# Optimization experiments

Measured on AMD Instinct MI355X. Metric: run time of the kernel, lower is better.

Reference implementation:

```python
import jax, jax.numpy as jnp
import numpy as np

HEADS = 16
D_MODEL = 1024
EXPANSION = 2
D_EXP = D_MODEL * EXPANSION          # 2048
D_HEAD = D_EXP // HEADS              # 128
B, SEQ = 1, 2048
LN_EPS = 1e-5
NEG_BIG = -1e10


def layer_norm(x, w, b):
    mu = jnp.mean(x, axis=-1, keepdims=True)
    var = jnp.var(x, axis=-1, keepdims=True)
    return (x - mu) * jax.lax.rsqrt(var + LN_EPS) * w + b


def setup_inputs() -> dict:
    key = jax.random.key(0)
    ks = jax.random.split(key, 8)
    d_out = 4 * D_EXP + HEADS  # merged fanout linear: q,k,v,p (D_EXP each) + y (HEADS)
    x = jax.random.normal(ks[0], (B, SEQ, D_MODEL), dtype=jnp.float32)
    W_in = 0.02 * jax.random.normal(ks[1], (d_out, D_MODEL), dtype=jnp.float32)
    b_in = jnp.zeros((d_out,), dtype=jnp.float32)
    # position head init from module: weight zeros, bias linspace(-8,8,heads)
    W_in = W_in.at[4 * D_EXP:].set(0.0)
    b_in = b_in.at[4 * D_EXP:].set(jnp.linspace(-8.0, 8.0, HEADS))
    W_out = 0.02 * (2 * 12) ** (-0.5) * jax.random.normal(ks[2], (D_MODEL, D_EXP), dtype=jnp.float32)
    in_ln_w = jnp.ones((D_MODEL,), dtype=jnp.float32)
    in_ln_b = jnp.zeros((D_MODEL,), dtype=jnp.float32)
    out_ln_w = jnp.ones((D_MODEL,), dtype=jnp.float32)
    out_ln_b = jnp.zeros((D_MODEL,), dtype=jnp.float32)
    smear_factor = jnp.linspace(-6.0, 6.0, HEADS)
    log_scale = jnp.zeros((HEADS,), dtype=jnp.float32)
    return {"x": x, "W_in": W_in, "b_in": b_in, "in_ln_w": in_ln_w, "in_ln_b": in_ln_b,
            "W_out": W_out, "out_ln_w": out_ln_w, "out_ln_b": out_ln_b,
            "smear_factor": smear_factor, "log_scale": log_scale}


def reference(x, W_in, b_in, in_ln_w, in_ln_b, W_out, out_ln_w, out_ln_b, smear_factor, log_scale):
    b, i, d = x.shape
    xn = layer_norm(x, in_ln_w, in_ln_b)
    proj = xn @ W_in.T + b_in  # [b, i, 4*D_EXP + HEADS]
    q, k, v, p, y = jnp.split(proj, [D_EXP, 2 * D_EXP, 3 * D_EXP, 4 * D_EXP], axis=-1)
    to_heads = lambda t: t.reshape(b, i, HEADS, D_HEAD).transpose(0, 2, 1, 3)  # b h i d
    q, k, v = to_heads(q), to_heads(k), to_heads(v)
    # smear mix: k_t <- (1-s)*k_t + s*k_{t-1}
    smear = jax.nn.sigmoid(smear_factor)[None, :, None, None]
    k_prev = jnp.pad(k, ((0, 0), (0, 0), (1, 0), (0, 0)))[:, :, :-1, :]
    k = (1 - smear) * k + smear * k_prev
    s = jnp.exp(log_scale)[None, :, None, None]
    # learned relative positions via cumulative sigmoid
    pos = jnp.cumsum(jax.nn.sigmoid(y).transpose(0, 2, 1), axis=-1)  # [b, h, i]
    relpos = pos[..., :, None] - pos[..., None, :]  # [b, h, i, i]
    causal = jnp.triu(jnp.full((i, i), NEG_BIG, dtype=x.dtype), k=1)
    mask = causal - relpos
    scores = jnp.einsum('bhid,bhjd->bhij', q / s, k / s) / np.sqrt(D_HEAD) + mask
    attn = jax.nn.softmax(scores, axis=-1)
    o = jnp.einsum('bhij,bhjd->bhid', attn, v)
    o = o.transpose(0, 2, 1, 3).reshape(b, i, D_EXP)  # b i (h d)
    out = (jax.nn.silu(p) * o) @ W_out.T
    return layer_norm(out, out_ln_w, out_ln_b)
```

## Files before the change

kernel.cpp:

```cpp
#include <hip/hip_runtime.h>
#include <hip/hip_bf16.h>
#include <cstdint>
#include <cstddef>

#define SEQ    2048
#define DMODEL 1024
#define DEXP   2048
#define NHEADS 16
#define DHEAD  128

typedef __bf16 bf16x8 __attribute__((ext_vector_type(8)));
typedef float  f32x4  __attribute__((ext_vector_type(4)));

__device__ __forceinline__ unsigned short f2bf(float f) {
  unsigned int u = __builtin_bit_cast(unsigned int, f);
  u = u + 0x7FFFu + ((u >> 16) & 1u);
  return (unsigned short)(u >> 16);
}
__device__ __forceinline__ float bf2f(unsigned short h) {
  unsigned int u = ((unsigned int)h) << 16;
  return __builtin_bit_cast(float, u);
}
__device__ __forceinline__ unsigned int pk2bf(float a, float b) {
  return ((unsigned int)f2bf(b) << 16) | f2bf(a);
}

__device__ __forceinline__ void gload_lds16(const void* g, void* l) {
  __builtin_amdgcn_global_load_lds(
      (const __attribute__((address_space(1))) unsigned int*)g,
      (__attribute__((address_space(3))) unsigned int*)l, 16, 0, 0);
}

__global__ __launch_bounds__(256) void ln_kernel(const float* __restrict__ in,
    const float* __restrict__ in2,
    const float* __restrict__ gw, const float* __restrict__ gb,
    unsigned short* __restrict__ out_bf, float* __restrict__ out_f) {
  int row = blockIdx.x, t = threadIdx.x;
  float4 v = reinterpret_cast<const float4*>(in + (size_t)row * DMODEL)[t];
  if (in2) {
    float4 v2 = reinterpret_cast<const float4*>(in2 + (size_t)row * DMODEL)[t];
    v.x += v2.x; v.y += v2.y; v.z += v2.z; v.w += v2.w;
  }
  float s  = v.x + v.y + v.z + v.w;
  float ss = v.x*v.x + v.y*v.y + v.z*v.z + v.w*v.w;
  #pragma unroll
  for (int m = 1; m < 64; m <<= 1) { s += __shfl_xor(s, m, 64); ss += __shfl_xor(ss, m, 64); }
  __shared__ float sh[8];
  if ((t & 63) == 0) { sh[t >> 6] = s; sh[4 + (t >> 6)] = ss; }
  __syncthreads();
  s  = sh[0] + sh[1] + sh[2] + sh[3];
  ss = sh[4] + sh[5] + sh[6] + sh[7];
  float mu  = s * (1.0f / DMODEL);
  float var = ss * (1.0f / DMODEL) - mu * mu;
  float rs  = rsqrtf(var + 1e-5f);
  float4 w4 = reinterpret_cast<const float4*>(gw)[t];
  float4 b4 = reinterpret_cast<const float4*>(gb)[t];
  float o0 = (v.x - mu) * rs * w4.x + b4.x;
  float o1 = (v.y - mu) * rs * w4.y + b4.y;
  float o2 = (v.z - mu) * rs * w4.z + b4.z;
  float o3 = (v.w - mu) * rs * w4.w + b4.w;
  if (out_bf) {
    unsigned short* op = out_bf + (size_t)row * DMODEL + t * 4;
    op[0] = f2bf(o0); op[1] = f2bf(o1); op[2] = f2bf(o2); op[3] = f2bf(o3);
  } else {
    float4 o4; o4.x = o0; o4.y = o1; o4.z = o2; o4.w = o3;
    reinterpret_cast<float4*>(out_f + (size_t)row * DMODEL)[t] = o4;
  }
}

__global__ void castboth(const float* __restrict__ in1, unsigned short* __restrict__ out1,
                         int n1, const float* __restrict__ in2,
                         unsigned short* __restrict__ out2, int n2) {
  int i = blockIdx.x * 256 + threadIdx.x;
  const float* in; unsigned short* out;
  if (i < n1) { in = in1; out = out1; }
  else { i -= n1; if (i >= n2) return; in = in2; out = out2; }
  float4 v = reinterpret_cast<const float4*>(in)[i];
  ushort4 o;
  o.x = f2bf(v.x); o.y = f2bf(v.y); o.z = f2bf(v.z); o.w = f2bf(v.w);
  reinterpret_cast<ushort4*>(out)[i] = o;
}

template<int EPI>
__global__ __launch_bounds__(256) void gemm_lds(
    const unsigned short* __restrict__ A, const unsigned short* __restrict__ B,
    int M, int N, int K,
    const float* __restrict__ b_in, const float* __restrict__ log_scale,
    unsigned short* __restrict__ outq, unsigned short* __restrict__ outk,
    unsigned short* __restrict__ outvt, unsigned short* __restrict__ outp,
    float* __restrict__ outf) {
  int nbn = N / 128;
  int tiles = (M / 128) * nbn;
  int bid = blockIdx.x;
  int part = 0;
  if constexpr (EPI == 1) { part = bid / tiles; bid -= part * tiles; }
  int bm = bid / nbn, bn = bid % nbn;
  int Klen = (EPI == 1) ? (K >> 1) : K;
  int koff = part * Klen;
  int tid = threadIdx.x;
  int wid = tid >> 6, l = tid & 63;
  int wr = wid >> 1, wc = wid & 1;
  int row0 = bm * 128, col0 = bn * 128;
  int c16 = l & 15, g = l >> 4;
  int srow = tid >> 3;
  int sch  = tid & 7;

  __shared__ __align__(16) char SMEM[65536];
  unsigned short* As0 = (unsigned short*)SMEM;
  unsigned short* Bs0 = (unsigned short*)(SMEM + 32768);
  unsigned short* vlds = (unsigned short*)SMEM;

  f32x4 acc[4][4];
  f32x4 z = {0.f, 0.f, 0.f, 0.f};
  #pragma unroll
  for (int i = 0; i < 4; ++i)
    #pragma unroll
    for (int j = 0; j < 4; ++j) acc[i][j] = z;

  auto STAGE = [&](int b, int kt) {
    int k0 = koff + kt * 64;
    #pragma unroll
    for (int rr = 0; rr < 4; ++rr) {
      int row = rr * 32 + srow;
      int kswz = k0 + ((sch ^ (row & 7)) * 8);
      gload_lds16(A + (size_t)(row0 + row) * K + kswz,
                  (char*)(As0 + b * 8192) + rr * 4096 + tid * 16);
      gload_lds16(B + (size_t)(col0 + row) * K + kswz,
                  (char*)(Bs0 + b * 8192) + rr * 4096 + tid * 16);
    }
  };

  int nkt = Klen >> 6;
  STAGE(0, 0);
  __syncthreads();

  for (int kt = 0; kt < nkt; ++kt) {
    int cur = kt & 1;
    if (kt + 1 < nkt) STAGE(cur ^ 1, kt + 1);
    const char* Ab = (const char*)(As0 + cur * 8192);
    const char* Bb = (const char*)(Bs0 + cur * 8192);
    int xo = (c16 & 7) << 4;
    #pragma unroll
    for (int ks = 0; ks < 2; ++ks) {
      bf16x8 a[4], b[4];
      #pragma unroll
      for (int i = 0; i < 4; ++i)
        a[i] = *reinterpret_cast<const bf16x8*>(
            Ab + (wr * 64 + i * 16 + c16) * 128 + ((ks * 64 + g * 16) ^ xo));
      #pragma unroll
      for (int j = 0; j < 4; ++j)
        b[j] = *reinterpret_cast<const bf16x8*>(
            Bb + (wc * 64 + j * 16 + c16) * 128 + ((ks * 64 + g * 16) ^ xo));
      __builtin_amdgcn_s_setprio(1);
      #pragma unroll
      for (int i = 0; i < 4; ++i)
        #pragma unroll
        for (int j = 0; j < 4; ++j)
          acc[i][j] = __builtin_amdgcn_mfma_f32_16x16x32_bf16(a[i], b[j], acc[i][j], 0, 0, 0);
      __builtin_amdgcn_s_setprio(0);
    }
    __syncthreads();
  }

  if constexpr (EPI == 0) {
    int sec = col0 >> 11;
    if (sec == 2) {
      #pragma unroll
      for (int i = 0; i < 4; ++i)
        #pragma unroll
        for (int j = 0; j < 4; ++j)
          #pragma unroll
          for (int r = 0; r < 4; ++r) {
            int lr = wr * 64 + i * 16 + g * 4 + r;
            int lc = wc * 64 + j * 16 + c16;
            vlds[lr * 130 + lc] = f2bf(acc[i][j][r] + b_in[col0 + lc]);
          }
      __syncthreads();
      int colv0 = col0 & 2047;
      int chunk = tid & 15;
      #pragma unroll
      for (int it = 0; it < 8; ++it) {
        int c = it * 16 + (tid >> 4);
        unsigned short tmp[8];
        #pragma unroll
        for (int e = 0; e < 8; ++e) tmp[e] = vlds[(chunk * 8 + e) * 130 + c];
        *reinterpret_cast<uint4*>(outvt + (size_t)(colv0 + c) * SEQ + row0 + chunk * 8) =
            *reinterpret_cast<const uint4*>(tmp);
      }
      return;
    }
  }

  #pragma unroll
  for (int i = 0; i < 4; ++i) {
    #pragma unroll
    for (int j = 0; j < 4; ++j) {
      #pragma unroll
      for (int r = 0; r < 4; ++r) {
        int gi = row0 + wr * 64 + i * 16 + g * 4 + r;
        int n  = col0 + wc * 64 + j * 16 + c16;
        float val = acc[i][j][r];
        if constexpr (EPI == 0) {
          val += b_in[n];
          int sec = n >> 11, nn = n & 2047, hh = nn >> 7;
          if (sec == 0) {
            float qs = __expf(-2.f * log_scale[hh]) * 0.088388347648318447f;
            outq[(size_t)gi * DEXP + nn] = f2bf(val * qs);
          } else if (sec == 1) {
            outk[(size_t)gi * DEXP + nn] = f2bf(val);
          } else {
            outp[(size_t)gi * DEXP + nn] = f2bf(val);
          }
        } else {
          outf[(size_t)part * M * N + (size_t)gi * N + n] = val;
        }
      }
    }
  }
}

__global__ __launch_bounds__(256) void yproj(const unsigned short* __restrict__ xn,
    const unsigned short* __restrict__ winbf, const float* __restrict__ b_in,
    float* __restrict__ sig_y) {
  int i = blockIdx.x;
  int t = threadIdx.x, wv = t >> 6, l = t & 63;
  const unsigned short* xr = xn + (size_t)i * DMODEL;
  for (int h = wv; h < NHEADS; h += 4) {
    const unsigned short* wr = winbf + (size_t)(4 * DEXP + h) * DMODEL;
    float s = 0.f;
    #pragma unroll
    for (int e = 0; e < 16; ++e) {
      int idx = l + 64 * e;
      s += bf2f(xr[idx]) * bf2f(wr[idx]);
    }
    #pragma unroll
    for (int m = 1; m < 64; m <<= 1) s += __shfl_xor(s, m, 64);
    if (l == 0) {
      float yv = s + b_in[4 * DEXP + h];
      sig_y[h * SEQ + i] = 1.f / (1.f + __expf(-yv));
    }
  }
}

__global__ __launch_bounds__(256) void scan_kernel(const float* __restrict__ sig_y,
                                                   float* __restrict__ pos) {
  int h = blockIdx.x, t = threadIdx.x;
  const float* in = sig_y + (size_t)h * SEQ;
  float v[8], s = 0.f;
  #pragma unroll
  for (int e = 0; e < 8; ++e) { v[e] = in[t * 8 + e]; s += v[e]; }
  __shared__ float sh[256];
  sh[t] = s;
  __syncthreads();
  for (int off = 1; off < 256; off <<= 1) {
    float add = (t >= off) ? sh[t - off] : 0.f;
    __syncthreads();
    sh[t] += add;
    __syncthreads();
  }
  float run = sh[t] - s;
  float* op = pos + (size_t)h * SEQ;
  #pragma unroll
  for (int e = 0; e < 8; ++e) { run += v[e]; op[t * 8 + e] = run; }
}

__global__ void smear_kernel(const unsigned short* __restrict__ projk,
    const float* __restrict__ smearf, unsigned short* __restrict__ ksm) {
  int idx = blockIdx.x * 256 + threadIdx.x;
  if (idx >= SEQ * DEXP) return;
  int i = idx >> 11, nn = idx & 2047, h = nn >> 7;
  float sf = 1.f / (1.f + __expf(-smearf[h]));
  float kc = bf2f(projk[idx]);
  float kp = (i > 0) ? bf2f(projk[idx - DEXP]) : 0.f;
  ksm[idx] = f2bf((1.f - sf) * kc + sf * kp);
}

__global__ __launch_bounds__(512) void attn_kernel(
    const unsigned short* __restrict__ q, const unsigned short* __restrict__ ksm,
    const unsigned short* __restrict__ vt, const unsigned short* __restrict__ projp,
    const float* __restrict__ pos, unsigned short* __restrict__ ap) {
  int bid = blockIdx.x;
  int swz = (bid & 7) * 64 + (bid >> 3);
  int h = swz >> 5;
  int low5 = swz & 31;
  int qc = (h & 1) ? (31 - low5) : low5;
  int q0 = qc * 64;
  int tid = threadIdx.x;
  int wid = tid >> 6, l = tid & 63;
  int w4 = wid & 3, jp = wid >> 2;
  int joff = jp * 32;
  int c16 = l & 15, g = l >> 4;

  __shared__ __align__(16) char SMEMa[65536];

  int qrow = q0 + w4 * 16 + c16;
  int wmax = q0 + w4 * 16 + 15;
  bf16x8 qf[4];
  {
    const unsigned short* qb = q + (size_t)qrow * DEXP + h * DHEAD + g * 8;
    #pragma unroll
    for (int f = 0; f < 4; ++f) qf[f] = *reinterpret_cast<const bf16x8*>(qb + f * 32);
  }
  float pos_q = pos[h * SEQ + qrow];
  float m_run = -1e30f, l_run = 0.f;
  f32x4 z = {0.f, 0.f, 0.f, 0.f};
  f32x4 oacc[8];
  #pragma unroll
  for (int d = 0; d < 8; ++d) oacc[d] = z;

  int ntiles = qc + 1;
  int kch = tid & 15;
  int vch = tid & 7;

  auto STAGE = [&](int b, int t) {
    int j0 = t * 64;
    {
      int row = (tid >> 4);
      #pragma unroll
      for (int rr = 0; rr < 2; ++rr) {
        int r2 = rr * 32 + row;
        gload_lds16(ksm + (size_t)(j0 + r2) * DEXP + h * DHEAD + ((kch ^ (r2 & 7)) * 8),
                    SMEMa + b * 16384 + rr * 8192 + tid * 16);
      }
    }
    {
      int row = (tid >> 3);
      #pragma unroll
      for (int rr = 0; rr < 2; ++rr) {
        int r2 = rr * 64 + row;
        gload_lds16(vt + (size_t)(h * DHEAD + r2) * SEQ + j0 + ((vch ^ (r2 & 7)) * 8),
                    SMEMa + 32768 + b * 16384 + rr * 8192 + tid * 16);
      }
    }
  };

  STAGE(0, 0);
  __syncthreads();

  for (int t = 0; t < ntiles; ++t) {
    int cur = t & 1;
    if (t + 1 < ntiles) STAGE(cur ^ 1, t + 1);
    int j0 = t * 64;
    if (j0 + joff <= wmax) {
      const char* Kb = SMEMa + cur * 16384;
      const char* Vb = SMEMa + 32768 + cur * 16384;
      f32x4 sT[2];
      #pragma unroll
      for (int sub = 0; sub < 2; ++sub) {
        sT[sub] = z;
        const char* kb = Kb + (joff + sub * 16 + c16) * 256;
        __builtin_amdgcn_s_setprio(1);
        #pragma unroll
        for (int f = 0; f < 4; ++f) {
          int cb = (f * 64 + g * 16) ^ ((c16 & 7) << 4);
          bf16x8 kf = *reinterpret_cast<const bf16x8*>(kb + cb);
          sT[sub] = __builtin_amdgcn_mfma_f32_16x16x32_bf16(kf, qf[f], sT[sub], 0, 0, 0);
        }
        __builtin_amdgcn_s_setprio(0);
      }
      float a[2][4], mt = -1e30f;
      #pragma unroll
      for (int sub = 0; sub < 2; ++sub) {
        float4 pjv = *reinterpret_cast<const float4*>(pos + h * SEQ + j0 + joff + sub * 16 + g * 4);
        float pj4[4] = { pjv.x, pjv.y, pjv.z, pjv.w };
        #pragma unroll
        for (int r = 0; r < 4; ++r) {
          int j = j0 + joff + sub * 16 + g * 4 + r;
          a[sub][r] = sT[sub][r] - pos_q + pj4[r] + (j > qrow ? -1e10f : 0.f);
          mt = fmaxf(mt, a[sub][r]);
        }
      }
      mt = fmaxf(mt, __shfl_xor(mt, 16, 64));
      mt = fmaxf(mt, __shfl_xor(mt, 32, 64));
      float mn = fmaxf(m_run, mt);
      if (mn - m_run > 8.f) {
        float alpha = __expf(m_run - mn);
        l_run *= alpha;
        #pragma unroll
        for (int d = 0; d < 8; ++d)
          #pragma unroll
          for (int r = 0; r < 4; ++r) oacc[d][r] *= alpha;
        m_run = mn;
      }
      float p[2][4];
      #pragma unroll
      for (int sub = 0; sub < 2; ++sub)
        #pragma unroll
        for (int r = 0; r < 4; ++r) { p[sub][r] = __expf(a[sub][r] - m_run); l_run += p[sub][r]; }
      unsigned long long pk0 = ((unsigned long long)pk2bf(p[0][2], p[0][3]) << 32)
                             |  pk2bf(p[0][0], p[0][1]);
      unsigned long long pk1 = ((unsigned long long)pk2bf(p[1][2], p[1][3]) << 32)
                             |  pk2bf(p[1][0], p[1][1]);
      int src = c16 + ((g & 1) << 5);
      unsigned long long t0 = __shfl(pk0, src, 64);
      unsigned long long t1 = __shfl(pk0, src + 16, 64);
      unsigned long long u0 = __shfl(pk1, src, 64);
      unsigned long long u1 = __shfl(pk1, src + 16, 64);
      union { unsigned long long u[2]; bf16x8 v; } pb;
      pb.u[0] = (g < 2) ? t0 : u0;
      pb.u[1] = (g < 2) ? t1 : u1;
      #pragma unroll
      for (int d = 0; d < 8; ++d) {
        const char* vb = Vb + (d * 16 + c16) * 128;
        int cb = (joff * 2 + g * 16) ^ ((c16 & 7) << 4);
        bf16x8 vf = *reinterpret_cast<const bf16x8*>(vb + cb);
        __builtin_amdgcn_s_setprio(1);
        oacc[d] = __builtin_amdgcn_mfma_f32_16x16x32_bf16(vf, pb.v, oacc[d], 0, 0, 0);
        __builtin_amdgcn_s_setprio(0);
      }
    }
    __syncthreads();
  }

  l_run += __shfl_xor(l_run, 16, 64);
  l_run += __shfl_xor(l_run, 32, 64);

  float* mbuf = (float*)SMEMa;
  float* obuf = (float*)(SMEMa + 1024);
  if (jp == 0) {
    if (g == 0) {
      mbuf[(w4 * 2 + 0) * 16 + c16] = m_run;
      mbuf[(w4 * 2 + 1) * 16 + c16] = l_run;
    }
    #pragma unroll
    for (int d = 0; d < 8; ++d)
      #pragma unroll
      for (int r = 0; r < 4; ++r)
        obuf[(w4 * 16 + c16) * 132 + d * 16 + g * 4 + r] = oacc[d][r];
  }
  __syncthreads();
  if (jp == 1) {
    float m0 = mbuf[(w4 * 2 + 0) * 16 + c16];
    float l0 = mbuf[(w4 * 2 + 1) * 16 + c16];
    float M = fmaxf(m0, m_run);
    float s0 = __expf(m0 - M), s1 = __expf(m_run - M);
    float invl = 1.0f / (l0 * s0 + l_run * s1);
    #pragma unroll
    for (int d = 0; d < 8; ++d) {
      int nn = h * DHEAD + d * 16 + g * 4;
      ushort4 pv4 = *reinterpret_cast<const ushort4*>(projp + (size_t)qrow * DEXP + nn);
      ushort4 o4;
      unsigned short* pvp = reinterpret_cast<unsigned short*>(&pv4);
      unsigned short* op  = reinterpret_cast<unsigned short*>(&o4);
      #pragma unroll
      for (int r = 0; r < 4; ++r) {
        float o = (obuf[(w4 * 16 + c16) * 132 + d * 16 + g * 4 + r] * s0 + oacc[d][r] * s1) * invl;
        float pv = bf2f(pvp[r]);
        float si = pv / (1.f + __expf(-pv));
        op[r] = f2bf(si * o);
      }
      *reinterpret_cast<ushort4*>(ap + (size_t)qrow * DEXP + nn) = o4;
    }
  }
}

extern "C" void kernel_launch(void* const* d_in, const int* in_sizes, int n_in,
                              void* d_out, int out_size, void* d_ws, size_t ws_size,
                              hipStream_t stream) {
  const float* x         = (const float*)d_in[0];
  const float* W_in      = (const float*)d_in[1];
  const float* b_in      = (const float*)d_in[2];
  const float* in_ln_w   = (const float*)d_in[3];
  const float* in_ln_b   = (const float*)d_in[4];
  const float* W_out     = (const float*)d_in[5];
  const float* out_ln_w  = (const float*)d_in[6];
  const float* out_ln_b  = (const float*)d_in[7];
  const float* smearf    = (const float*)d_in[8];
  const float* log_scale = (const float*)d_in[9];
  float* out = (float*)d_out;

  char* ws = (char*)d_ws;
  size_t off = 0;
  auto alloc = [&](size_t bytes) -> void* {
    void* p = ws + off;
    off += (bytes + 255) & ~(size_t)255;
    return p;
  };
  unsigned short* xn     = (unsigned short*)alloc((size_t)SEQ * DMODEL * 2);
  unsigned short* winbf  = (unsigned short*)alloc((size_t)(4 * DEXP + NHEADS) * DMODEL * 2);
  unsigned short* woutbf = (unsigned short*)alloc((size_t)DMODEL * DEXP * 2);
  unsigned short* projq  = (unsigned short*)alloc((size_t)SEQ * DEXP * 2);
  unsigned short* projk  = (unsigned short*)alloc((size_t)SEQ * DEXP * 2);
  unsigned short* projp  = (unsigned short*)alloc((size_t)SEQ * DEXP * 2);
  unsigned short* vtb    = (unsigned short*)alloc((size_t)SEQ * DEXP * 2);
  unsigned short* ksm    = (unsigned short*)alloc((size_t)SEQ * DEXP * 2);
  unsigned short* apb    = (unsigned short*)alloc((size_t)SEQ * DEXP * 2);
  float* sig_y = (float*)alloc((size_t)NHEADS * SEQ * 4);
  float* posb  = (float*)alloc((size_t)NHEADS * SEQ * 4);
  float* outf  = (float*)alloc((size_t)2 * SEQ * DMODEL * 4);

  int nwin4  = (4 * DEXP + NHEADS) * DMODEL / 4;
  int nwout4 = DMODEL * DEXP / 4;
  castboth<<<(nwin4 + nwout4 + 255) / 256, 256, 0, stream>>>(
      W_in, winbf, nwin4, W_out, woutbf, nwout4);
  ln_kernel<<<SEQ, 256, 0, stream>>>(x, nullptr, in_ln_w, in_ln_b, xn, nullptr);
  gemm_lds<0><<<(SEQ / 128) * (4 * DEXP / 128), 256, 0, stream>>>(
      xn, winbf, SEQ, 4 * DEXP, DMODEL, b_in, log_scale, projq, projk, vtb, projp, nullptr);
  yproj<<<SEQ, 256, 0, stream>>>(xn, winbf, b_in, sig_y);
  scan_kernel<<<NHEADS, 256, 0, stream>>>(sig_y, posb);
  smear_kernel<<<(SEQ * DEXP + 255) / 256, 256, 0, stream>>>(projk, smearf, ksm);
  attn_kernel<<<512, 512, 0, stream>>>(projq, ksm, vtb, projp, posb, apb);
  gemm_lds<1><<<2 * (SEQ / 128) * (DMODEL / 128), 256, 0, stream>>>(
      apb, woutbf, SEQ, DMODEL, DEXP, nullptr, nullptr, nullptr, nullptr, nullptr, nullptr, outf);
  ln_kernel<<<SEQ, 256, 0, stream>>>(outf, outf + (size_t)SEQ * DMODEL, out_ln_w, out_ln_b,
                                     nullptr, out);
}
```

Baseline: 164.8 us.

## Split attention KV tile across four wave groups with 1024-thread blocks

The attention block grows from 8 to 16 waves, so each wave group handles a 16-key slice of every 64-key tile instead of 32 keys. Staging now takes one load per thread for K and V. Partial softmax states are combined in a tree-style merge through shared memory before the final silu-gated write. This aims for more latency hiding and parallelism per block. In exchange, half of each PV MFMA operand is zeros, more barriers are needed, and the launch bound rises to 1024 threads, which may cap registers per thread.

```diff
diff --git a/kernel.cpp b/kernel.cpp
--- a/kernel.cpp
+++ b/kernel.cpp
@@ -275,7 +275,7 @@
   ksm[idx] = f2bf((1.f - sf) * kc + sf * kp);
 }
 
-__global__ __launch_bounds__(512) void attn_kernel(
+__global__ __launch_bounds__(1024, 8) void attn_kernel(
     const unsigned short* __restrict__ q, const unsigned short* __restrict__ ksm,
     const unsigned short* __restrict__ vt, const unsigned short* __restrict__ projp,
     const float* __restrict__ pos, unsigned short* __restrict__ ap) {
@@ -287,8 +287,8 @@
   int q0 = qc * 64;
   int tid = threadIdx.x;
   int wid = tid >> 6, l = tid & 63;
-  int w4 = wid & 3, jp = wid >> 2;
-  int joff = jp * 32;
+  int w4 = wid & 3, jq = wid >> 2;
+  int joff = jq * 16;
   int c16 = l & 15, g = l >> 4;
 
   __shared__ __align__(16) char SMEMa[65536];
@@ -315,22 +315,14 @@
   auto STAGE = [&](int b, int t) {
     int j0 = t * 64;
     {
-      int row = (tid >> 4);
-      #pragma unroll
-      for (int rr = 0; rr < 2; ++rr) {
-        int r2 = rr * 32 + row;
-        gload_lds16(ksm + (size_t)(j0 + r2) * DEXP + h * DHEAD + ((kch ^ (r2 & 7)) * 8),
-                    SMEMa + b * 16384 + rr * 8192 + tid * 16);
-      }
+      int row = tid >> 4;
+      gload_lds16(ksm + (size_t)(j0 + row) * DEXP + h * DHEAD + ((kch ^ (row & 7)) * 8),
+                  SMEMa + b * 16384 + tid * 16);
     }
     {
-      int row = (tid >> 3);
-      #pragma unroll
-      for (int rr = 0; rr < 2; ++rr) {
-        int r2 = rr * 64 + row;
-        gload_lds16(vt + (size_t)(h * DHEAD + r2) * SEQ + j0 + ((vch ^ (r2 & 7)) * 8),
-                    SMEMa + 32768 + b * 16384 + rr * 8192 + tid * 16);
-      }
+      int row = tid >> 3;
+      gload_lds16(vt + (size_t)(h * DHEAD + row) * SEQ + j0 + ((vch ^ (row & 7)) * 8),
+                  SMEMa + 32768 + b * 16384 + tid * 16);
     }
   };
 
@@ -344,31 +336,24 @@
     if (j0 + joff <= wmax) {
       const char* Kb = SMEMa + cur * 16384;
       const char* Vb = SMEMa + 32768 + cur * 16384;
-      f32x4 sT[2];
-      #pragma unroll
-      for (int sub = 0; sub < 2; ++sub) {
-        sT[sub] = z;
-        const char* kb = Kb + (joff + sub * 16 + c16) * 256;
-        __builtin_amdgcn_s_setprio(1);
-        #pragma unroll
-        for (int f = 0; f < 4; ++f) {
-          int cb = (f * 64 + g * 16) ^ ((c16 & 7) << 4);
-          bf16x8 kf = *reinterpret_cast<const bf16x8*>(kb + cb);
-          sT[sub] = __builtin_amdgcn_mfma_f32_16x16x32_bf16(kf, qf[f], sT[sub], 0, 0, 0);
-        }
-        __builtin_amdgcn_s_setprio(0);
-      }
-      float a[2][4], mt = -1e30f;
-      #pragma unroll
-      for (int sub = 0; sub < 2; ++sub) {
-        float4 pjv = *reinterpret_cast<const float4*>(pos + h * SEQ + j0 + joff + sub * 16 + g * 4);
-        float pj4[4] = { pjv.x, pjv.y, pjv.z, pjv.w };
-        #pragma unroll
-        for (int r = 0; r < 4; ++r) {
-          int j = j0 + joff + sub * 16 + g * 4 + r;
-          a[sub][r] = sT[sub][r] - pos_q + pj4[r] + (j > qrow ? -1e10f : 0.f);
-          mt = fmaxf(mt, a[sub][r]);
-        }
+      f32x4 sT = z;
+      const char* kb = Kb + (joff + c16) * 256;
+      __builtin_amdgcn_s_setprio(1);
+      #pragma unroll
+      for (int f = 0; f < 4; ++f) {
+        int cb = (f * 64 + g * 16) ^ ((c16 & 7) << 4);
+        bf16x8 kf = *reinterpret_cast<const bf16x8*>(kb + cb);
+        sT = __builtin_amdgcn_mfma_f32_16x16x32_bf16(kf, qf[f], sT, 0, 0, 0);
+      }
+      __builtin_amdgcn_s_setprio(0);
+      float a4[4], mt = -1e30f;
+      float4 pjv = *reinterpret_cast<const float4*>(pos + h * SEQ + j0 + joff + g * 4);
+      float pj4[4] = { pjv.x, pjv.y, pjv.z, pjv.w };
+      #pragma unroll
+      for (int r = 0; r < 4; ++r) {
+        int j = j0 + joff + g * 4 + r;
+        a4[r] = sT[r] - pos_q + pj4[r] + (j > qrow ? -1e10f : 0.f);
+        mt = fmaxf(mt, a4[r]);
       }
       mt = fmaxf(mt, __shfl_xor(mt, 16, 64));
       mt = fmaxf(mt, __shfl_xor(mt, 32, 64));
@@ -382,27 +367,22 @@
           for (int r = 0; r < 4; ++r) oacc[d][r] *= alpha;
         m_run = mn;
       }
-      float p[2][4];
-      #pragma unroll
-      for (int sub = 0; sub < 2; ++sub)
-        #pragma unroll
-        for (int r = 0; r < 4; ++r) { p[sub][r] = __expf(a[sub][r] - m_run); l_run += p[sub][r]; }
-      unsigned long long pk0 = ((unsigned long long)pk2bf(p[0][2], p[0][3]) << 32)
-                             |  pk2bf(p[0][0], p[0][1]);
-      unsigned long long pk1 = ((unsigned long long)pk2bf(p[1][2], p[1][3]) << 32)
-                             |  pk2bf(p[1][0], p[1][1]);
+      float p4[4];
+      #pragma unroll
+      for (int r = 0; r < 4; ++r) { p4[r] = __expf(a4[r] - m_run); l_run += p4[r]; }
+      unsigned long long pk = ((unsigned long long)pk2bf(p4[2], p4[3]) << 32)
+                            |  pk2bf(p4[0], p4[1]);
       int src = c16 + ((g & 1) << 5);
-      unsigned long long t0 = __shfl(pk0, src, 64);
-      unsigned long long t1 = __shfl(pk0, src + 16, 64);
-      unsigned long long u0 = __shfl(pk1, src, 64);
-      unsigned long long u1 = __shfl(pk1, src + 16, 64);
+      unsigned long long u0 = __shfl(pk, src, 64);
+      unsigned long long u1 = __shfl(pk, src + 16, 64);
       union { unsigned long long u[2]; bf16x8 v; } pb;
-      pb.u[0] = (g < 2) ? t0 : u0;
-      pb.u[1] = (g < 2) ? t1 : u1;
+      pb.u[0] = (g < 2) ? u0 : 0ull;
+      pb.u[1] = (g < 2) ? u1 : 0ull;
+      int gg = g & 1;
       #pragma unroll
       for (int d = 0; d < 8; ++d) {
         const char* vb = Vb + (d * 16 + c16) * 128;
-        int cb = (joff * 2 + g * 16) ^ ((c16 & 7) << 4);
+        int cb = (joff * 2 + gg * 16) ^ ((c16 & 7) << 4);
         bf16x8 vf = *reinterpret_cast<const bf16x8*>(vb + cb);
         __builtin_amdgcn_s_setprio(1);
         oacc[d] = __builtin_amdgcn_mfma_f32_16x16x32_bf16(vf, pb.v, oacc[d], 0, 0, 0);
@@ -414,10 +394,12 @@
 
   l_run += __shfl_xor(l_run, 16, 64);
   l_run += __shfl_xor(l_run, 32, 64);
-
-  float* mbuf = (float*)SMEMa;
-  float* obuf = (float*)(SMEMa + 1024);
-  if (jp == 0) {
+  __syncthreads();
+
+  float* obuf = (float*)SMEMa;
+  float* mbuf = (float*)(SMEMa + 33792);
+
+  auto WRITE = [&]() {
     if (g == 0) {
       mbuf[(w4 * 2 + 0) * 16 + c16] = m_run;
       mbuf[(w4 * 2 + 1) * 16 + c16] = l_run;
@@ -427,14 +409,34 @@
       #pragma unroll
       for (int r = 0; r < 4; ++r)
         obuf[(w4 * 16 + c16) * 132 + d * 16 + g * 4 + r] = oacc[d][r];
-  }
-  __syncthreads();
-  if (jp == 1) {
-    float m0 = mbuf[(w4 * 2 + 0) * 16 + c16];
-    float l0 = mbuf[(w4 * 2 + 1) * 16 + c16];
-    float M = fmaxf(m0, m_run);
-    float s0 = __expf(m0 - M), s1 = __expf(m_run - M);
-    float invl = 1.0f / (l0 * s0 + l_run * s1);
+  };
+  auto MERGE = [&]() {
+    float mB = mbuf[(w4 * 2 + 0) * 16 + c16];
+    float lB = mbuf[(w4 * 2 + 1) * 16 + c16];
+    float M = fmaxf(m_run, mB);
+    float sA = __expf(m_run - M), sB = __expf(mB - M);
+    #pragma unroll
+    for (int d = 0; d < 8; ++d)
+      #pragma unroll
+      for (int r = 0; r < 4; ++r)
+        oacc[d][r] = oacc[d][r] * sA + obuf[(w4 * 16 + c16) * 132 + d * 16 + g * 4 + r] * sB;
+    l_run = l_run * sA + lB * sB;
+    m_run = M;
+  };
+
+  if (jq == 1) WRITE();
+  __syncthreads();
+  if (jq == 0) MERGE();
+  __syncthreads();
+  if (jq == 3) WRITE();
+  __syncthreads();
+  if (jq == 2) MERGE();
+  __syncthreads();
+  if (jq == 2) WRITE();
+  __syncthreads();
+  if (jq == 0) {
+    MERGE();
+    float inv_l = 1.0f / l_run;
     #pragma unroll
     for (int d = 0; d < 8; ++d) {
       int nn = h * DHEAD + d * 16 + g * 4;
@@ -444,7 +446,7 @@
       unsigned short* op  = reinterpret_cast<unsigned short*>(&o4);
       #pragma unroll
       for (int r = 0; r < 4; ++r) {
-        float o = (obuf[(w4 * 16 + c16) * 132 + d * 16 + g * 4 + r] * s0 + oacc[d][r] * s1) * invl;
+        float o = oacc[d][r] * inv_l;
         float pv = bf2f(pvp[r]);
         float si = pv / (1.f + __expf(-pv));
         op[r] = f2bf(si * o);
@@ -499,7 +501,7 @@
   yproj<<<SEQ, 256, 0, stream>>>(xn, winbf, b_in, sig_y);
   scan_kernel<<<NHEADS, 256, 0, stream>>>(sig_y, posb);
   smear_kernel<<<(SEQ * DEXP + 255) / 256, 256, 0, stream>>>(projk, smearf, ksm);
-  attn_kernel<<<512, 512, 0, stream>>>(projq, ksm, vtb, projp, posb, apb);
+  attn_kernel<<<512, 1024, 0, stream>>>(projq, ksm, vtb, projp, posb, apb);
   gemm_lds<1><<<2 * (SEQ / 128) * (DMODEL / 128), 256, 0, stream>>>(
       apb, woutbf, SEQ, DMODEL, DEXP, nullptr, nullptr, nullptr, nullptr, nullptr, nullptr, outf);
   ln_kernel<<<SEQ, 256, 0, stream>>>(outf, outf + (size_t)SEQ * DMODEL, out_ln_w, out_ln_b,
```

Result: slower. 262.4 us (+59.2%).

## Load V directly from global in attention and split output GEMM K four ways

Applied to the files above, without the earlier changes.

The attention kernel stops staging V tiles in LDS. Each lane now reads its V fragments straight from global memory, which shrinks shared memory from 64KB to 35KB and should allow more blocks per CU, but the V reads become strided and uncoalesced. Separately, the output GEMM splits K into four parts instead of two, giving four times as many blocks, and the final layer norm sums four partial buffers. That adds extra partial-sum traffic in exchange for more parallelism in the output projection.

```diff
diff --git a/kernel.cpp b/kernel.cpp
--- a/kernel.cpp
+++ b/kernel.cpp
@@ -32,7 +32,8 @@
 }
 
 __global__ __launch_bounds__(256) void ln_kernel(const float* __restrict__ in,
-    const float* __restrict__ in2,
+    const float* __restrict__ in2, const float* __restrict__ in3,
+    const float* __restrict__ in4,
     const float* __restrict__ gw, const float* __restrict__ gb,
     unsigned short* __restrict__ out_bf, float* __restrict__ out_f) {
   int row = blockIdx.x, t = threadIdx.x;
@@ -40,6 +41,14 @@
   if (in2) {
     float4 v2 = reinterpret_cast<const float4*>(in2 + (size_t)row * DMODEL)[t];
     v.x += v2.x; v.y += v2.y; v.z += v2.z; v.w += v2.w;
+  }
+  if (in3) {
+    float4 v3 = reinterpret_cast<const float4*>(in3 + (size_t)row * DMODEL)[t];
+    v.x += v3.x; v.y += v3.y; v.z += v3.z; v.w += v3.w;
+  }
+  if (in4) {
+    float4 v4 = reinterpret_cast<const float4*>(in4 + (size_t)row * DMODEL)[t];
+    v.x += v4.x; v.y += v4.y; v.z += v4.z; v.w += v4.w;
   }
   float s  = v.x + v.y + v.z + v.w;
   float ss = v.x*v.x + v.y*v.y + v.z*v.z + v.w*v.w;
@@ -95,7 +104,7 @@
   int part = 0;
   if constexpr (EPI == 1) { part = bid / tiles; bid -= part * tiles; }
   int bm = bid / nbn, bn = bid % nbn;
-  int Klen = (EPI == 1) ? (K >> 1) : K;
+  int Klen = (EPI == 1) ? (K >> 2) : K;
   int koff = part * Klen;
   int tid = threadIdx.x;
   int wid = tid >> 6, l = tid & 63;
@@ -291,7 +300,7 @@
   int joff = jp * 32;
   int c16 = l & 15, g = l >> 4;
 
-  __shared__ __align__(16) char SMEMa[65536];
+  __shared__ __align__(16) char SMEMa[35840];
 
   int qrow = q0 + w4 * 16 + c16;
   int wmax = q0 + w4 * 16 + 15;
@@ -310,27 +319,15 @@
 
   int ntiles = qc + 1;
   int kch = tid & 15;
-  int vch = tid & 7;
 
   auto STAGE = [&](int b, int t) {
     int j0 = t * 64;
-    {
-      int row = (tid >> 4);
-      #pragma unroll
-      for (int rr = 0; rr < 2; ++rr) {
-        int r2 = rr * 32 + row;
-        gload_lds16(ksm + (size_t)(j0 + r2) * DEXP + h * DHEAD + ((kch ^ (r2 & 7)) * 8),
-                    SMEMa + b * 16384 + rr * 8192 + tid * 16);
-      }
-    }
-    {
-      int row = (tid >> 3);
-      #pragma unroll
-      for (int rr = 0; rr < 2; ++rr) {
-        int r2 = rr * 64 + row;
-        gload_lds16(vt + (size_t)(h * DHEAD + r2) * SEQ + j0 + ((vch ^ (r2 & 7)) * 8),
-                    SMEMa + 32768 + b * 16384 + rr * 8192 + tid * 16);
-      }
+    int row = (tid >> 4);
+    #pragma unroll
+    for (int rr = 0; rr < 2; ++rr) {
+      int r2 = rr * 32 + row;
+      gload_lds16(ksm + (size_t)(j0 + r2) * DEXP + h * DHEAD + ((kch ^ (r2 & 7)) * 8),
+                  SMEMa + b * 16384 + rr * 8192 + tid * 16);
     }
   };
 
@@ -343,7 +340,6 @@
     int j0 = t * 64;
     if (j0 + joff <= wmax) {
       const char* Kb = SMEMa + cur * 16384;
-      const char* Vb = SMEMa + 32768 + cur * 16384;
       f32x4 sT[2];
       #pragma unroll
       for (int sub = 0; sub < 2; ++sub) {
@@ -399,11 +395,10 @@
       union { unsigned long long u[2]; bf16x8 v; } pb;
       pb.u[0] = (g < 2) ? t0 : u0;
       pb.u[1] = (g < 2) ? t1 : u1;
+      const unsigned short* vbase = vt + (size_t)(h * DHEAD + c16) * SEQ + j0 + joff + g * 8;
       #pragma unroll
       for (int d = 0; d < 8; ++d) {
-        const char* vb = Vb + (d * 16 + c16) * 128;
-        int cb = (joff * 2 + g * 16) ^ ((c16 & 7) << 4);
-        bf16x8 vf = *reinterpret_cast<const bf16x8*>(vb + cb);
+        bf16x8 vf = *reinterpret_cast<const bf16x8*>(vbase + (size_t)(d * 16) * SEQ);
         __builtin_amdgcn_s_setprio(1);
         oacc[d] = __builtin_amdgcn_mfma_f32_16x16x32_bf16(vf, pb.v, oacc[d], 0, 0, 0);
         __builtin_amdgcn_s_setprio(0);
@@ -487,21 +482,23 @@
   unsigned short* apb    = (unsigned short*)alloc((size_t)SEQ * DEXP * 2);
   float* sig_y = (float*)alloc((size_t)NHEADS * SEQ * 4);
   float* posb  = (float*)alloc((size_t)NHEADS * SEQ * 4);
-  float* outf  = (float*)alloc((size_t)2 * SEQ * DMODEL * 4);
+  float* outf  = (float*)alloc((size_t)4 * SEQ * DMODEL * 4);
 
   int nwin4  = (4 * DEXP + NHEADS) * DMODEL / 4;
   int nwout4 = DMODEL * DEXP / 4;
   castboth<<<(nwin4 + nwout4 + 255) / 256, 256, 0, stream>>>(
       W_in, winbf, nwin4, W_out, woutbf, nwout4);
-  ln_kernel<<<SEQ, 256, 0, stream>>>(x, nullptr, in_ln_w, in_ln_b, xn, nullptr);
+  ln_kernel<<<SEQ, 256, 0, stream>>>(x, nullptr, nullptr, nullptr,
+                                     in_ln_w, in_ln_b, xn, nullptr);
   gemm_lds<0><<<(SEQ / 128) * (4 * DEXP / 128), 256, 0, stream>>>(
       xn, winbf, SEQ, 4 * DEXP, DMODEL, b_in, log_scale, projq, projk, vtb, projp, nullptr);
   yproj<<<SEQ, 256, 0, stream>>>(xn, winbf, b_in, sig_y);
   scan_kernel<<<NHEADS, 256, 0, stream>>>(sig_y, posb);
   smear_kernel<<<(SEQ * DEXP + 255) / 256, 256, 0, stream>>>(projk, smearf, ksm);
   attn_kernel<<<512, 512, 0, stream>>>(projq, ksm, vtb, projp, posb, apb);
-  gemm_lds<1><<<2 * (SEQ / 128) * (DMODEL / 128), 256, 0, stream>>>(
+  gemm_lds<1><<<4 * (SEQ / 128) * (DMODEL / 128), 256, 0, stream>>>(
       apb, woutbf, SEQ, DMODEL, DEXP, nullptr, nullptr, nullptr, nullptr, nullptr, nullptr, outf);
-  ln_kernel<<<SEQ, 256, 0, stream>>>(outf, outf + (size_t)SEQ * DMODEL, out_ln_w, out_ln_b,
-                                     nullptr, out);
-}
+  size_t mn = (size_t)SEQ * DMODEL;
+  ln_kernel<<<SEQ, 256, 0, stream>>>(outf, outf + mn, outf + 2 * mn, outf + 3 * mn,
+                                     out_ln_w, out_ln_b, nullptr, out);
+}
```

Result: slower. 224.7 us (+36.3%).
